# Kernel optimization log

Measured on AMD Instinct MI355X. Metric: run time of the kernel, lower is better.

Reference implementation:

```python
import jax, jax.numpy as jnp
import numpy as np

IN_FEATS = 602
N_HIDDEN = 256
N_CLASSES = 41
N_SRC0 = 292864   # block-1 src nodes (2-hop neighborhood)
N_DST0 = 11264    # block-1 dst == block-0 src (1-hop neighborhood)
N_DST1 = 1024     # seeds
FAN0 = 25         # neighbors per dst in block applied by layer 0
FAN1 = 10         # neighbors per dst in block applied by layer 1


def setup_inputs() -> dict:
    key = jax.random.key(0)
    ks = jax.random.split(key, 9)
    x = jax.random.normal(ks[0], (N_SRC0, IN_FEATS), dtype=jnp.float32)
    src_idx0 = jax.random.randint(ks[1], (N_DST0 * FAN0,), 0, N_SRC0)
    src_idx1 = jax.random.randint(ks[2], (N_DST1 * FAN1,), 0, N_DST0)
    s0 = 1.0 / np.sqrt(IN_FEATS)
    s1 = 1.0 / np.sqrt(N_HIDDEN)
    W_self0 = jax.random.uniform(ks[3], (IN_FEATS, N_HIDDEN), jnp.float32, -s0, s0)
    W_neigh0 = jax.random.uniform(ks[4], (IN_FEATS, N_HIDDEN), jnp.float32, -s0, s0)
    b0 = jnp.zeros((N_HIDDEN,), jnp.float32)
    W_self1 = jax.random.uniform(ks[5], (N_HIDDEN, N_CLASSES), jnp.float32, -s1, s1)
    W_neigh1 = jax.random.uniform(ks[6], (N_HIDDEN, N_CLASSES), jnp.float32, -s1, s1)
    b1 = jnp.zeros((N_CLASSES,), jnp.float32)
    return {"x": x, "W_self0": W_self0, "W_neigh0": W_neigh0, "b0": b0,
            "W_self1": W_self1, "W_neigh1": W_neigh1, "b1": b1,
            "src_idx0": src_idx0, "src_idx1": src_idx1}


def _sage_layer(h_src, h_dst, src_idx, fanout, W_self, W_neigh, b):
    # mean aggregation over exactly `fanout` sampled neighbors per dst node
    n_dst = h_dst.shape[0]
    h_neigh = h_src[src_idx].reshape(n_dst, fanout, -1).mean(axis=1)
    return h_dst @ W_self + h_neigh @ W_neigh + b


def reference(x, W_self0, W_neigh0, b0, W_self1, W_neigh1, b1, src_idx0, src_idx1):
    # layer 0: [N_SRC0, in] -> [N_DST0, hidden], relu; dropout is identity (eval mode)
    h = jax.nn.relu(_sage_layer(x, x[:N_DST0], src_idx0, FAN0, W_self0, W_neigh0, b0))
    # layer 1: [N_DST0, hidden] -> [N_DST1, classes], no activation
    out = _sage_layer(h, h[:N_DST1], src_idx1, FAN1, W_self1, W_neigh1, b1)
    return out
```

## Files before the change

kernel.cpp:

```cpp
#include <hip/hip_runtime.h>
#include <hip/hip_bf16.h>

#define IN_FEATS 602
#define N_HIDDEN 256
#define N_CLASSES 41
#define N_SRC0 292864
#define N_DST0 11264
#define N_DST1 1024
#define FAN0 25
#define FAN1 10
#define KPAD 1216
#define LDSW 72
#define NCHUNK 4
#define CH (N_DST0 / NCHUNK)
#define NW ((KPAD / 32) * 8)
#define NGC (4 * (CH / 64))
#define NAC (CH / 4)

typedef __attribute__((ext_vector_type(4))) float f32x4;
typedef __attribute__((ext_vector_type(8))) short bf16x8;

static __device__ __forceinline__ unsigned pack_bf16x2(float lo, float hi) {
    unsigned a = __float_as_uint(lo);
    unsigned b = __float_as_uint(hi);
    a = (a + 0x7fffu + ((a >> 16) & 1u)) >> 16;
    b = (b + 0x7fffu + ((b >> 16) & 1u)) >> 16;
    return (a & 0xffffu) | (b << 16);
}

#define SMBYTES (2 * 64 * LDSW * 2)

static __device__ __forceinline__ void wprep_role(
    int b, char* sm,
    const float* __restrict__ Ws, const float* __restrict__ Wn,
    __hip_bfloat16* __restrict__ Wt)
{
    float (*tile)[33] = (float(*)[33])sm;
    const int k0 = (b % (KPAD / 32)) * 32;
    const int n0 = (b / (KPAD / 32)) * 32;
    const int tx = threadIdx.x & 31, ty = threadIdx.x >> 5;

    #pragma unroll
    for (int i = 0; i < 4; ++i) {
        const int k = k0 + ty + i * 8;
        const int n = n0 + tx;
        float v = 0.f;
        if (k < IN_FEATS)            v = Ws[(size_t)k * N_HIDDEN + n];
        else if (k < 2 * IN_FEATS)   v = Wn[(size_t)(k - IN_FEATS) * N_HIDDEN + n];
        tile[ty + i * 8][tx] = v;
    }
    __syncthreads();
    #pragma unroll
    for (int i = 0; i < 4; ++i) {
        const int n = n0 + ty + i * 8;
        const int k = k0 + tx;
        Wt[(size_t)n * KPAD + k] = __float2bfloat16(tile[tx][ty + i * 8]);
    }
}

static __device__ __forceinline__ void agg_role(
    int b, int dst0, char* sm,
    const float* __restrict__ x,
    const int* __restrict__ idx0,
    __hip_bfloat16* __restrict__ A)
{
    int (*sidx)[FAN0] = (int(*)[FAN0])sm;
    const int wave = threadIdx.x >> 6;
    const int lane = threadIdx.x & 63;
    const int d = dst0 + b * 4 + wave;

    if (lane < FAN0) sidx[wave][lane] = idx0[d * FAN0 + lane];
    __syncthreads();

    unsigned* Aself = (unsigned*)(A + (size_t)d * KPAD);
    const float* xself = x + (size_t)d * IN_FEATS;

    if (lane < 6) Aself[602 + lane] = 0u;

    #pragma unroll
    for (int p = 0; p < 5; ++p) {
        const int f2 = p * 64 + lane;
        if (f2 <= 300) {
            const int f = f2 * 2;
            float sx = 0.f, sy = 0.f;
            #pragma unroll
            for (int n = 0; n < FAN0; ++n) {
                const float2 v = *(const float2*)&x[(size_t)sidx[wave][n] * IN_FEATS + f];
                sx += v.x; sy += v.y;
            }
            const float2 sv = *(const float2*)&xself[f];
            *(unsigned*)((char*)Aself + f2 * 4) = pack_bf16x2(sv.x, sv.y);
            *(unsigned*)((char*)Aself + 1204 + f2 * 4) =
                pack_bf16x2(sx * (1.0f / FAN0), sy * (1.0f / FAN0));
        }
    }
}

static __device__ __forceinline__ void gemm_role(
    int b, int dst0, char* sm,
    const __hip_bfloat16* __restrict__ A,
    const __hip_bfloat16* __restrict__ Wt,
    const float* __restrict__ bias,
    float* __restrict__ h)
{
    short* As = (short*)sm;
    short* Bs = As + 64 * LDSW;

    const int tid  = threadIdx.x;
    const int lane = tid & 63;
    const int wave = tid >> 6;
    const int wm = wave >> 1, wn = wave & 1;
    const int g = lane >> 4, r = lane & 15;
    const int n0 = (b & 3) * 64;
    const int m0 = dst0 + (b >> 2) * 64;

    const int srow = tid >> 2;
    const int sc   = (tid & 3) * 16;

    const size_t a_off = (size_t)(m0 + srow) * KPAD + sc;
    const size_t b_off = (size_t)(n0 + srow) * KPAD + sc;

    f32x4 acc[2][2] = {};

    for (int k0 = 0; k0 < KPAD; k0 += 64) {
        *(float4*)&As[srow * LDSW + sc]     = *(const float4*)&A[a_off + k0];
        *(float4*)&As[srow * LDSW + sc + 8] = *(const float4*)&A[a_off + k0 + 8];
        *(float4*)&Bs[srow * LDSW + sc]     = *(const float4*)&Wt[b_off + k0];
        *(float4*)&Bs[srow * LDSW + sc + 8] = *(const float4*)&Wt[b_off + k0 + 8];
        __syncthreads();

        #pragma unroll
        for (int kh = 0; kh < 2; ++kh) {
            const bf16x8 af0 = *(const bf16x8*)&As[(wm * 32 +      r) * LDSW + kh * 32 + g * 8];
            const bf16x8 af1 = *(const bf16x8*)&As[(wm * 32 + 16 + r) * LDSW + kh * 32 + g * 8];
            const bf16x8 bf0 = *(const bf16x8*)&Bs[(wn * 32 +      r) * LDSW + kh * 32 + g * 8];
            const bf16x8 bf1 = *(const bf16x8*)&Bs[(wn * 32 + 16 + r) * LDSW + kh * 32 + g * 8];

            acc[0][0] = __builtin_amdgcn_mfma_f32_16x16x32_bf16(af0, bf0, acc[0][0], 0, 0, 0);
            acc[0][1] = __builtin_amdgcn_mfma_f32_16x16x32_bf16(af0, bf1, acc[0][1], 0, 0, 0);
            acc[1][0] = __builtin_amdgcn_mfma_f32_16x16x32_bf16(af1, bf0, acc[1][0], 0, 0, 0);
            acc[1][1] = __builtin_amdgcn_mfma_f32_16x16x32_bf16(af1, bf1, acc[1][1], 0, 0, 0);
        }
        __syncthreads();
    }

    #pragma unroll
    for (int mh = 0; mh < 2; ++mh)
        #pragma unroll
        for (int nh = 0; nh < 2; ++nh) {
            const int col = n0 + wn * 32 + nh * 16 + r;
            const float bv = bias[col];
            #pragma unroll
            for (int j = 0; j < 4; ++j) {
                const int row = m0 + wm * 32 + mh * 16 + g * 4 + j;
                h[(size_t)row * N_HIDDEN + col] = fmaxf(acc[mh][nh][j] + bv, 0.f);
            }
        }
}

__global__ __launch_bounds__(256) void combo_kernel(
    const float* __restrict__ x,
    const int* __restrict__ idx0,
    const float* __restrict__ Ws0,
    const float* __restrict__ Wn0,
    const float* __restrict__ b0,
    __hip_bfloat16* __restrict__ A,
    __hip_bfloat16* __restrict__ Wt,
    float* __restrict__ h,
    int nw, int ng, int gemm_dst0, int agg_dst0)
{
    __shared__ __align__(16) char sm[SMBYTES];
    int b = blockIdx.x;
    if (b < nw) { wprep_role(b, sm, Ws0, Wn0, Wt); return; }
    b -= nw;
    if (b < ng) { gemm_role(b, gemm_dst0, sm, A, Wt, b0, h); return; }
    b -= ng;
    agg_role(b, agg_dst0, sm, x, idx0, A);
}

__global__ __launch_bounds__(256) void tail_kernel(
    const float* __restrict__ h,
    const int* __restrict__ idx1,
    const float* __restrict__ Ws,
    const float* __restrict__ Wn,
    const float* __restrict__ b,
    float* __restrict__ out)
{
    const int w = threadIdx.x >> 6;
    const int lane = threadIdx.x & 63;
    const int d = blockIdx.x * 4 + w;

    __shared__ float hd[4][N_HIDDEN];
    __shared__ float hn[4][N_HIDDEN];
    __shared__ int sidx[4][FAN1];
    if (lane < FAN1) sidx[w][lane] = idx1[d * FAN1 + lane];
    __syncthreads();

    {
        const int k0 = lane * 4;
        const float4 self = *(const float4*)&h[(size_t)d * N_HIDDEN + k0];
        float ax = 0.f, ay = 0.f, az = 0.f, aw = 0.f;
        #pragma unroll
        for (int i = 0; i < FAN1; ++i) {
            const float4 v = *(const float4*)&h[(size_t)sidx[w][i] * N_HIDDEN + k0];
            ax += v.x; ay += v.y; az += v.z; aw += v.w;
        }
        *(float4*)&hd[w][k0] = self;
        hn[w][k0 + 0] = ax * (1.0f / FAN1);
        hn[w][k0 + 1] = ay * (1.0f / FAN1);
        hn[w][k0 + 2] = az * (1.0f / FAN1);
        hn[w][k0 + 3] = aw * (1.0f / FAN1);
    }
    __syncthreads();

    if (lane < N_CLASSES) {
        const int n = lane;
        float a0 = b[n], a1 = 0.f, a2 = 0.f, a3 = 0.f;
        #pragma unroll 4
        for (int k = 0; k < N_HIDDEN; k += 4) {
            a0 += hd[w][k + 0] * Ws[(k + 0) * N_CLASSES + n] + hn[w][k + 0] * Wn[(k + 0) * N_CLASSES + n];
            a1 += hd[w][k + 1] * Ws[(k + 1) * N_CLASSES + n] + hn[w][k + 1] * Wn[(k + 1) * N_CLASSES + n];
            a2 += hd[w][k + 2] * Ws[(k + 2) * N_CLASSES + n] + hn[w][k + 2] * Wn[(k + 2) * N_CLASSES + n];
            a3 += hd[w][k + 3] * Ws[(k + 3) * N_CLASSES + n] + hn[w][k + 3] * Wn[(k + 3) * N_CLASSES + n];
        }
        out[(size_t)d * N_CLASSES + n] = a0 + a1 + a2 + a3;
    }
}

extern "C" void kernel_launch(void* const* d_in, const int* in_sizes, int n_in,
                              void* d_out, int out_size, void* d_ws, size_t ws_size,
                              hipStream_t stream) {
    const float* x       = (const float*)d_in[0];
    const float* Wself0  = (const float*)d_in[1];
    const float* Wneigh0 = (const float*)d_in[2];
    const float* b0      = (const float*)d_in[3];
    const float* Wself1  = (const float*)d_in[4];
    const float* Wneigh1 = (const float*)d_in[5];
    const float* b1      = (const float*)d_in[6];
    const int*   idx0    = (const int*)d_in[7];
    const int*   idx1    = (const int*)d_in[8];
    float* out = (float*)d_out;

    __hip_bfloat16* A  = (__hip_bfloat16*)d_ws;
    __hip_bfloat16* Wt = A + (size_t)N_DST0 * KPAD;
    float*          h  = (float*)(Wt + (size_t)N_HIDDEN * KPAD);

    combo_kernel<<<NW + NAC, 256, 0, stream>>>(
        x, idx0, Wself0, Wneigh0, b0, A, Wt, h, NW, 0, 0, 0);
    for (int c = 1; c < NCHUNK; ++c)
        combo_kernel<<<NGC + NAC, 256, 0, stream>>>(
            x, idx0, Wself0, Wneigh0, b0, A, Wt, h,
            0, NGC, (c - 1) * CH, c * CH);
    combo_kernel<<<NGC, 256, 0, stream>>>(
        x, idx0, Wself0, Wneigh0, b0, A, Wt, h, 0, NGC, (NCHUNK - 1) * CH, 0);
    tail_kernel<<<N_DST1 / 4, 256, 0, stream>>>(h, idx1, Wself1, Wneigh1, b1, out);
}
```

Before: 238.5 us.

## Project all source rows through neighbor weights before gathering and averaging

Reorders layer 0 so that every source node is multiplied by W_neigh first, in one large bf16 MFMA GEMM that reads x directly, and only then are the 256-wide bf16 projections gathered and averaged per destination. The self term is computed the same way for the destination rows. This replaces the random 602-float row gathers and the chunked aggregate/GEMM pipeline with a streaming read of all of x plus a narrower gather. In exchange it does GEMM work on every source row, including rows no destination samples, writes a large bf16 intermediate, and adds a second bf16 rounding step.

Measured after the change: 462.9 us. 94.1% more time.

```diff
diff --git a/kernel.cpp b/kernel.cpp
--- a/kernel.cpp
+++ b/kernel.cpp
@@ -2,6 +2,7 @@
 #include <hip/hip_bf16.h>
 
 #define IN_FEATS 602
+#define KP 608
 #define N_HIDDEN 256
 #define N_CLASSES 41
 #define N_SRC0 292864
@@ -9,13 +10,8 @@
 #define N_DST1 1024
 #define FAN0 25
 #define FAN1 10
-#define KPAD 1216
-#define LDSW 72
-#define NCHUNK 4
-#define CH (N_DST0 / NCHUNK)
-#define NW ((KPAD / 32) * 8)
-#define NGC (4 * (CH / 64))
-#define NAC (CH / 4)
+#define NBLK_N (N_SRC0 / 128)
+#define NBLK_S (N_DST0 / 128)
 
 typedef __attribute__((ext_vector_type(4))) float f32x4;
 typedef __attribute__((ext_vector_type(8))) short bf16x8;
@@ -28,154 +24,146 @@
     return (a & 0xffffu) | (b << 16);
 }
 
-#define SMBYTES (2 * 64 * LDSW * 2)
-
-static __device__ __forceinline__ void wprep_role(
-    int b, char* sm,
+__global__ __launch_bounds__(256) void wprep_kernel(
     const float* __restrict__ Ws, const float* __restrict__ Wn,
-    __hip_bfloat16* __restrict__ Wt)
-{
-    float (*tile)[33] = (float(*)[33])sm;
-    const int k0 = (b % (KPAD / 32)) * 32;
-    const int n0 = (b / (KPAD / 32)) * 32;
+    __hip_bfloat16* __restrict__ Wst, __hip_bfloat16* __restrict__ Wnt)
+{
+    const float* W = blockIdx.z ? Wn : Ws;
+    __hip_bfloat16* Wt = blockIdx.z ? Wnt : Wst;
+
+    __shared__ float tile[32][33];
+    const int k0 = blockIdx.x * 32, n0 = blockIdx.y * 32;
     const int tx = threadIdx.x & 31, ty = threadIdx.x >> 5;
 
     #pragma unroll
     for (int i = 0; i < 4; ++i) {
         const int k = k0 + ty + i * 8;
         const int n = n0 + tx;
-        float v = 0.f;
-        if (k < IN_FEATS)            v = Ws[(size_t)k * N_HIDDEN + n];
-        else if (k < 2 * IN_FEATS)   v = Wn[(size_t)(k - IN_FEATS) * N_HIDDEN + n];
-        tile[ty + i * 8][tx] = v;
+        tile[ty + i * 8][tx] = (k < IN_FEATS) ? W[(size_t)k * N_HIDDEN + n] : 0.f;
     }
     __syncthreads();
     #pragma unroll
     for (int i = 0; i < 4; ++i) {
         const int n = n0 + ty + i * 8;
         const int k = k0 + tx;
-        Wt[(size_t)n * KPAD + k] = __float2bfloat16(tile[tx][ty + i * 8]);
-    }
-}
-
-static __device__ __forceinline__ void agg_role(
-    int b, int dst0, char* sm,
+        Wt[(size_t)n * KP + k] = __float2bfloat16(tile[tx][ty + i * 8]);
+    }
+}
+
+__global__ __launch_bounds__(512, 4) void zgemm_kernel(
     const float* __restrict__ x,
-    const int* __restrict__ idx0,
-    __hip_bfloat16* __restrict__ A)
-{
-    int (*sidx)[FAN0] = (int(*)[FAN0])sm;
-    const int wave = threadIdx.x >> 6;
-    const int lane = threadIdx.x & 63;
-    const int d = dst0 + b * 4 + wave;
-
-    if (lane < FAN0) sidx[wave][lane] = idx0[d * FAN0 + lane];
-    __syncthreads();
-
-    unsigned* Aself = (unsigned*)(A + (size_t)d * KPAD);
-    const float* xself = x + (size_t)d * IN_FEATS;
-
-    if (lane < 6) Aself[602 + lane] = 0u;
-
-    #pragma unroll
-    for (int p = 0; p < 5; ++p) {
-        const int f2 = p * 64 + lane;
-        if (f2 <= 300) {
-            const int f = f2 * 2;
-            float sx = 0.f, sy = 0.f;
-            #pragma unroll
-            for (int n = 0; n < FAN0; ++n) {
-                const float2 v = *(const float2*)&x[(size_t)sidx[wave][n] * IN_FEATS + f];
-                sx += v.x; sy += v.y;
-            }
-            const float2 sv = *(const float2*)&xself[f];
-            *(unsigned*)((char*)Aself + f2 * 4) = pack_bf16x2(sv.x, sv.y);
-            *(unsigned*)((char*)Aself + 1204 + f2 * 4) =
-                pack_bf16x2(sx * (1.0f / FAN0), sy * (1.0f / FAN0));
-        }
-    }
-}
-
-static __device__ __forceinline__ void gemm_role(
-    int b, int dst0, char* sm,
-    const __hip_bfloat16* __restrict__ A,
-    const __hip_bfloat16* __restrict__ Wt,
-    const float* __restrict__ bias,
-    float* __restrict__ h)
-{
-    short* As = (short*)sm;
-    short* Bs = As + 64 * LDSW;
+    const __hip_bfloat16* __restrict__ Wnt,
+    const __hip_bfloat16* __restrict__ Wst,
+    __hip_bfloat16* __restrict__ zn,
+    __hip_bfloat16* __restrict__ zs)
+{
+    __shared__ short As[128 * 40];
+    __shared__ short Bs[256 * 40];
+
+    const int bb = blockIdx.x;
+    const __hip_bfloat16* Wt = (bb < NBLK_N) ? Wnt : Wst;
+    __hip_bfloat16* zout      = (bb < NBLK_N) ? zn  : zs;
+    const int m0 = ((bb < NBLK_N) ? bb : bb - NBLK_N) * 128;
 
     const int tid  = threadIdx.x;
     const int lane = tid & 63;
-    const int wave = tid >> 6;
-    const int wm = wave >> 1, wn = wave & 1;
-    const int g = lane >> 4, r = lane & 15;
-    const int n0 = (b & 3) * 64;
-    const int m0 = dst0 + (b >> 2) * 64;
-
-    const int srow = tid >> 2;
-    const int sc   = (tid & 3) * 16;
-
-    const size_t a_off = (size_t)(m0 + srow) * KPAD + sc;
-    const size_t b_off = (size_t)(n0 + srow) * KPAD + sc;
-
-    f32x4 acc[2][2] = {};
-
-    for (int k0 = 0; k0 < KPAD; k0 += 64) {
-        *(float4*)&As[srow * LDSW + sc]     = *(const float4*)&A[a_off + k0];
-        *(float4*)&As[srow * LDSW + sc + 8] = *(const float4*)&A[a_off + k0 + 8];
-        *(float4*)&Bs[srow * LDSW + sc]     = *(const float4*)&Wt[b_off + k0];
-        *(float4*)&Bs[srow * LDSW + sc + 8] = *(const float4*)&Wt[b_off + k0 + 8];
+    const int w    = tid >> 6;
+    const int wm   = w >> 2;
+    const int wn   = w & 3;
+    const int r    = lane & 15;
+    const int g    = lane >> 4;
+
+    const int arow = tid >> 2;
+    const int akq  = (tid & 3) * 8;
+    const int brow = tid >> 1;
+    const int bkq  = (tid & 1) * 16;
+
+    const float* xrow = x + (size_t)(m0 + arow) * IN_FEATS;
+
+    f32x4 acc[4][4] = {};
+
+    for (int k0 = 0; k0 < KP; k0 += 32) {
+        float2 av[4];
+        #pragma unroll
+        for (int i = 0; i < 4; ++i) {
+            const int k = k0 + akq + i * 2;
+            av[i] = (k < IN_FEATS) ? *(const float2*)&xrow[k] : make_float2(0.f, 0.f);
+        }
+        const float4 bv0 = *(const float4*)&Wt[(size_t)brow * KP + k0 + bkq];
+        const float4 bv1 = *(const float4*)&Wt[(size_t)brow * KP + k0 + bkq + 8];
+
         __syncthreads();
 
-        #pragma unroll
-        for (int kh = 0; kh < 2; ++kh) {
-            const bf16x8 af0 = *(const bf16x8*)&As[(wm * 32 +      r) * LDSW + kh * 32 + g * 8];
-            const bf16x8 af1 = *(const bf16x8*)&As[(wm * 32 + 16 + r) * LDSW + kh * 32 + g * 8];
-            const bf16x8 bf0 = *(const bf16x8*)&Bs[(wn * 32 +      r) * LDSW + kh * 32 + g * 8];
-            const bf16x8 bf1 = *(const bf16x8*)&Bs[(wn * 32 + 16 + r) * LDSW + kh * 32 + g * 8];
-
-            acc[0][0] = __builtin_amdgcn_mfma_f32_16x16x32_bf16(af0, bf0, acc[0][0], 0, 0, 0);
-            acc[0][1] = __builtin_amdgcn_mfma_f32_16x16x32_bf16(af0, bf1, acc[0][1], 0, 0, 0);
-            acc[1][0] = __builtin_amdgcn_mfma_f32_16x16x32_bf16(af1, bf0, acc[1][0], 0, 0, 0);
-            acc[1][1] = __builtin_amdgcn_mfma_f32_16x16x32_bf16(af1, bf1, acc[1][1], 0, 0, 0);
-        }
+        uint4 ap;
+        ap.x = pack_bf16x2(av[0].x, av[0].y);
+        ap.y = pack_bf16x2(av[1].x, av[1].y);
+        ap.z = pack_bf16x2(av[2].x, av[2].y);
+        ap.w = pack_bf16x2(av[3].x, av[3].y);
+        *(uint4*)&As[arow * 40 + akq] = ap;
+        *(float4*)&Bs[brow * 40 + bkq]     = bv0;
+        *(float4*)&Bs[brow * 40 + bkq + 8] = bv1;
+
         __syncthreads();
-    }
-
-    #pragma unroll
-    for (int mh = 0; mh < 2; ++mh)
-        #pragma unroll
-        for (int nh = 0; nh < 2; ++nh) {
-            const int col = n0 + wn * 32 + nh * 16 + r;
-            const float bv = bias[col];
+
+        bf16x8 bf[4];
+        #pragma unroll
+        for (int nf = 0; nf < 4; ++nf)
+            bf[nf] = *(const bf16x8*)&Bs[(wn * 64 + nf * 16 + r) * 40 + g * 8];
+        #pragma unroll
+        for (int mf = 0; mf < 4; ++mf) {
+            const bf16x8 af = *(const bf16x8*)&As[(wm * 64 + mf * 16 + r) * 40 + g * 8];
+            #pragma unroll
+            for (int nf = 0; nf < 4; ++nf)
+                acc[mf][nf] = __builtin_amdgcn_mfma_f32_16x16x32_bf16(af, bf[nf], acc[mf][nf], 0, 0, 0);
+        }
+    }
+
+    #pragma unroll
+    for (int mf = 0; mf < 4; ++mf)
+        #pragma unroll
+        for (int nf = 0; nf < 4; ++nf) {
+            const int col = wn * 64 + nf * 16 + r;
             #pragma unroll
             for (int j = 0; j < 4; ++j) {
-                const int row = m0 + wm * 32 + mh * 16 + g * 4 + j;
-                h[(size_t)row * N_HIDDEN + col] = fmaxf(acc[mh][nh][j] + bv, 0.f);
+                const int row = m0 + wm * 64 + mf * 16 + g * 4 + j;
+                zout[(size_t)row * N_HIDDEN + col] = __float2bfloat16(acc[mf][nf][j]);
             }
         }
 }
 
-__global__ __launch_bounds__(256) void combo_kernel(
-    const float* __restrict__ x,
+__global__ __launch_bounds__(256) void zfin_kernel(
+    const __hip_bfloat16* __restrict__ zn,
+    const __hip_bfloat16* __restrict__ zs,
     const int* __restrict__ idx0,
-    const float* __restrict__ Ws0,
-    const float* __restrict__ Wn0,
     const float* __restrict__ b0,
-    __hip_bfloat16* __restrict__ A,
-    __hip_bfloat16* __restrict__ Wt,
-    float* __restrict__ h,
-    int nw, int ng, int gemm_dst0, int agg_dst0)
-{
-    __shared__ __align__(16) char sm[SMBYTES];
-    int b = blockIdx.x;
-    if (b < nw) { wprep_role(b, sm, Ws0, Wn0, Wt); return; }
-    b -= nw;
-    if (b < ng) { gemm_role(b, gemm_dst0, sm, A, Wt, b0, h); return; }
-    b -= ng;
-    agg_role(b, agg_dst0, sm, x, idx0, A);
+    float* __restrict__ h)
+{
+    const int w = threadIdx.x >> 6;
+    const int lane = threadIdx.x & 63;
+    const int d = blockIdx.x * 4 + w;
+
+    __shared__ int sidx[4][FAN0];
+    if (lane < FAN0) sidx[w][lane] = idx0[d * FAN0 + lane];
+    __syncthreads();
+
+    float s0 = 0.f, s1 = 0.f, s2 = 0.f, s3 = 0.f;
+    #pragma unroll
+    for (int n = 0; n < FAN0; ++n) {
+        const uint2 v = *(const uint2*)&zn[(size_t)sidx[w][n] * N_HIDDEN + lane * 4];
+        s0 += __uint_as_float(v.x << 16);
+        s1 += __uint_as_float(v.x & 0xffff0000u);
+        s2 += __uint_as_float(v.y << 16);
+        s3 += __uint_as_float(v.y & 0xffff0000u);
+    }
+    const uint2 sv = *(const uint2*)&zs[(size_t)d * N_HIDDEN + lane * 4];
+    const float4 bv = *(const float4*)&b0[lane * 4];
+
+    float4 o;
+    o.x = fmaxf(__uint_as_float(sv.x << 16)          + s0 * (1.0f / FAN0) + bv.x, 0.f);
+    o.y = fmaxf(__uint_as_float(sv.x & 0xffff0000u)  + s1 * (1.0f / FAN0) + bv.y, 0.f);
+    o.z = fmaxf(__uint_as_float(sv.y << 16)          + s2 * (1.0f / FAN0) + bv.z, 0.f);
+    o.w = fmaxf(__uint_as_float(sv.y & 0xffff0000u)  + s3 * (1.0f / FAN0) + bv.w, 0.f);
+    *(float4*)&h[(size_t)d * N_HIDDEN + lane * 4] = o;
 }
 
 __global__ __launch_bounds__(256) void tail_kernel(
@@ -241,17 +229,14 @@
     const int*   idx1    = (const int*)d_in[8];
     float* out = (float*)d_out;
 
-    __hip_bfloat16* A  = (__hip_bfloat16*)d_ws;
-    __hip_bfloat16* Wt = A + (size_t)N_DST0 * KPAD;
-    float*          h  = (float*)(Wt + (size_t)N_HIDDEN * KPAD);
-
-    combo_kernel<<<NW + NAC, 256, 0, stream>>>(
-        x, idx0, Wself0, Wneigh0, b0, A, Wt, h, NW, 0, 0, 0);
-    for (int c = 1; c < NCHUNK; ++c)
-        combo_kernel<<<NGC + NAC, 256, 0, stream>>>(
-            x, idx0, Wself0, Wneigh0, b0, A, Wt, h,
-            0, NGC, (c - 1) * CH, c * CH);
-    combo_kernel<<<NGC, 256, 0, stream>>>(
-        x, idx0, Wself0, Wneigh0, b0, A, Wt, h, 0, NGC, (NCHUNK - 1) * CH, 0);
+    __hip_bfloat16* zn  = (__hip_bfloat16*)d_ws;
+    __hip_bfloat16* zs  = zn + (size_t)N_SRC0 * N_HIDDEN;
+    float*          h   = (float*)(zs + (size_t)N_DST0 * N_HIDDEN);
+    __hip_bfloat16* Wst = (__hip_bfloat16*)(h + (size_t)N_DST0 * N_HIDDEN);
+    __hip_bfloat16* Wnt = Wst + (size_t)N_HIDDEN * KP;
+
+    wprep_kernel<<<dim3(KP / 32, N_HIDDEN / 32, 2), 256, 0, stream>>>(Wself0, Wneigh0, Wst, Wnt);
+    zgemm_kernel<<<NBLK_N + NBLK_S, 512, 0, stream>>>(x, Wnt, Wst, zn, zs);
+    zfin_kernel<<<N_DST0 / 4, 256, 0, stream>>>(zn, zs, idx0, b0, h);
     tail_kernel<<<N_DST1 / 4, 256, 0, stream>>>(h, idx1, Wself1, Wneigh1, b1, out);
 }
```
